# Kernel optimization log

Hardware: AMD Instinct MI355X
Metric: run time of the kernel (lower is better)

The kernel has to match this reference:

```python
import jax, jax.numpy as jnp
import numpy as np

NUM_HEADS = 16

def _rope_tables(seq_len, dim, dtype):
    # LongLlamaRotaryEmbedding: inv_freq = 1/10000^(2i/d), emb = cat(freqs, freqs)
    inv_freq = 1.0 / (10000.0 ** (jnp.arange(0, dim, 2, dtype=jnp.float32) / dim))
    t = jnp.arange(seq_len, dtype=jnp.float32)
    freqs = t[:, None] * inv_freq[None, :]            # [S, D/2]
    emb = jnp.concatenate([freqs, freqs], axis=-1)    # [S, D]
    return jnp.cos(emb).astype(dtype), jnp.sin(emb).astype(dtype)

def _rotate_half(x):
    x1, x2 = jnp.split(x, 2, axis=-1)
    return jnp.concatenate([-x2, x1], axis=-1)

def _rotate_one(x, cos, sin, pos):
    # x: [B,H,S,D]; pos: [B,S] int -> gather-indexed RoPE
    c = cos[pos][:, None, :, :]  # [B,1,S,D]
    s = sin[pos][:, None, :, :]
    return x * c + _rotate_half(x) * s

def setup_inputs() -> dict:
    key = jax.random.key(0)
    B, S, HID = 1, 4096, 2048
    ks = jax.random.split(key, 5)
    hidden_states = jax.random.normal(ks[0], (B, S, HID), dtype=jnp.float32)
    # causal additive mask [B,1,S,S]: 0 where allowed, large negative above diagonal
    causal = jnp.tril(jnp.ones((S, S), dtype=bool))
    attention_mask = jnp.where(causal, 0.0, -1e9).astype(jnp.float32)[None, None]
    attention_mask = jnp.broadcast_to(attention_mask, (B, 1, S, S))
    position_ids = jnp.broadcast_to(jnp.arange(S, dtype=jnp.int64), (B, S))
    scale = 0.02
    Wq = jax.random.normal(ks[1], (HID, HID), dtype=jnp.float32) * scale
    Wk = jax.random.normal(ks[2], (HID, HID), dtype=jnp.float32) * scale
    Wv = jax.random.normal(ks[3], (HID, HID), dtype=jnp.float32) * scale
    Wo = jax.random.normal(ks[4], (HID, HID), dtype=jnp.float32) * scale
    return {"hidden_states": hidden_states, "attention_mask": attention_mask,
            "position_ids": position_ids, "Wq": Wq, "Wk": Wk, "Wv": Wv, "Wo": Wo}

def reference(hidden_states, attention_mask, position_ids, Wq, Wk, Wv, Wo):
    B, S, HID = hidden_states.shape
    H = NUM_HEADS
    D = HID // H
    # QKV projections (torch Linear: y = x @ W.T), shaped [B,H,S,D]
    q = (hidden_states @ Wq.T).reshape(B, S, H, D).transpose(0, 2, 1, 3)
    k = (hidden_states @ Wk.T).reshape(B, S, H, D).transpose(0, 2, 1, 3)
    v = (hidden_states @ Wv.T).reshape(B, S, H, D).transpose(0, 2, 1, 3)
    kv_seq_len = k.shape[-2]
    cos, sin = _rope_tables(kv_seq_len, D, hidden_states.dtype)
    # rel_pos_ids = position_ids - min over seq (gather-indexed RoPE)
    rel = position_ids - jnp.min(position_ids, axis=-1, keepdims=True)
    q = _rotate_one(q, cos, sin, rel[:, -S:])
    k = _rotate_one(k, cos, sin, rel)
    scores = jnp.einsum('bhqd,bhkd->bhqk', q, k) / jnp.asarray(np.sqrt(D), hidden_states.dtype)
    scores = scores + attention_mask  # additive mask broadcast over heads
    attn = jax.nn.softmax(scores, axis=-1)
    out = jnp.einsum('bhqk,bhkd->bhqd', attn, v)
    out = out.transpose(0, 2, 1, 3).reshape(B, S, HID)
    return out @ Wo.T
```

## Files before the change

### kernel.cpp

```cpp
#include <hip/hip_runtime.h>
#include <stdint.h>

typedef uint16_t u16;
typedef __bf16 bf16x8 __attribute__((ext_vector_type(8)));
typedef float f32x4 __attribute__((ext_vector_type(4)));
typedef uint32_t u32x4 __attribute__((ext_vector_type(4)));

__device__ __forceinline__ u16 f2bf(float f) {
    uint32_t u = __builtin_bit_cast(uint32_t, f);
    u += 0x7fffu + ((u >> 16) & 1u);
    return (u16)(u >> 16);
}
__device__ __forceinline__ float bf2f(u16 h) {
    uint32_t u = ((uint32_t)h) << 16;
    return __builtin_bit_cast(float, u);
}

__global__ __launch_bounds__(256) void cvt_f32_bf16(const float* __restrict__ in,
                                                    u16* __restrict__ out, int n4) {
    int i = blockIdx.x * 256 + threadIdx.x;
    if (i >= n4) return;
    float4 v = ((const float4*)in)[i];
    u16 o[4] = { f2bf(v.x), f2bf(v.y), f2bf(v.z), f2bf(v.w) };
    *(uint64_t*)(out + 4 * (size_t)i) = *(const uint64_t*)o;
}

__global__ __launch_bounds__(256) void cvt_w4(const float* __restrict__ W0,
                                              const float* __restrict__ W1,
                                              const float* __restrict__ W2,
                                              const float* __restrict__ W3,
                                              u16* __restrict__ Wqkv,
                                              u16* __restrict__ Wob) {
    int b = blockIdx.x;
    int w = b >> 12;
    const float* in = (w == 0 ? W0 : w == 1 ? W1 : w == 2 ? W2 : W3);
    u16* out = (w < 3 ? Wqkv + (size_t)w * 4194304 : Wob);
    int i = (b & 4095) * 256 + threadIdx.x;
    float4 v = ((const float4*)in)[i];
    u16 o[4] = { f2bf(v.x), f2bf(v.y), f2bf(v.z), f2bf(v.w) };
    *(uint64_t*)(out + 4 * (size_t)i) = *(const uint64_t*)o;
}

__device__ __forceinline__ void gload16(const u16* g, u16* l) {
    __builtin_amdgcn_global_load_lds(
        (const __attribute__((address_space(1))) void*)g,
        (__attribute__((address_space(3))) void*)l, 16, 0, 0);
}

__global__ __launch_bounds__(512, 1) void gemm_qkv(const u16* __restrict__ A,
                                                   const u16* __restrict__ B,
                                                   u16* __restrict__ Cq,
                                                   int K) {
    __shared__ u16 As[2][16384];
    __shared__ u16 Bs[2][16384];
    const int tid  = threadIdx.x;
    const int wave = tid >> 6, lane = tid & 63;
    const int quad = lane >> 4, ln = lane & 15;
    const int wm = wave >> 2, wn = wave & 3;
    const int bm = blockIdx.x, bn = blockIdx.y;
    const int NT = K >> 6;
    const u16* Ab = A + (size_t)bm * 256 * K;
    const u16* Bb = B + (size_t)bn * 256 * K;
    const int lr  = lane >> 3;
    const int lc8 = ((lane & 7) ^ lr) * 8;
    const int sw  = ln & 7;
    const int cA0 = ((0 + quad) ^ sw) * 8;
    const int cA1 = ((4 + quad) ^ sw) * 8;

    f32x4 acc[8][4] = {};

    auto stage_a = [&](int t, int q) {
        int ch = q * 8 + wave;
        gload16(Ab + (size_t)(ch * 8 + lr) * K + t * 64 + lc8, &As[t & 1][ch * 512]);
    };
    auto stage_b = [&](int t, int q) {
        int ch = q * 8 + wave;
        gload16(Bb + (size_t)(ch * 8 + lr) * K + t * 64 + lc8, &Bs[t & 1][ch * 512]);
    };

    for (int q = 0; q < 4; q++) stage_a(0, q);
    for (int q = 0; q < 4; q++) stage_b(0, q);
    for (int q = 0; q < 4; q++) stage_a(1, q);
    asm volatile("s_waitcnt vmcnt(4)" ::: "memory");
    __builtin_amdgcn_s_barrier();

    for (int t = 0; t < NT; ++t) {
        const u16* Asb = As[t & 1];
        const u16* Bsb = Bs[t & 1];
        bf16x8 a0[8], a1[8], b0[4], b1[4];
#pragma unroll
        for (int i = 0; i < 8; i++)
            a0[i] = *(const bf16x8*)(Asb + (wm * 128 + i * 16 + ln) * 64 + cA0);
#pragma unroll
        for (int j = 0; j < 4; j++)
            b0[j] = *(const bf16x8*)(Bsb + (wn * 64 + j * 16 + ln) * 64 + cA0);
        if (t + 1 < NT) { stage_b(t + 1, 0); stage_b(t + 1, 1); }
        __builtin_amdgcn_s_barrier();
        asm volatile("s_waitcnt lgkmcnt(0)" ::: "memory");
        __builtin_amdgcn_s_setprio(1);
#pragma unroll
        for (int i = 0; i < 4; i++)
#pragma unroll
            for (int j = 0; j < 4; j++)
                acc[i][j] = __builtin_amdgcn_mfma_f32_16x16x32_bf16(a0[i], b0[j], acc[i][j], 0, 0, 0);
        __builtin_amdgcn_s_setprio(0);
        __builtin_amdgcn_s_barrier();
#pragma unroll
        for (int i = 0; i < 8; i++)
            a1[i] = *(const bf16x8*)(Asb + (wm * 128 + i * 16 + ln) * 64 + cA1);
        if (t + 1 < NT) { stage_b(t + 1, 2); stage_b(t + 1, 3); }
        __builtin_amdgcn_s_barrier();
        asm volatile("s_waitcnt lgkmcnt(0)" ::: "memory");
        __builtin_amdgcn_s_setprio(1);
#pragma unroll
        for (int i = 4; i < 8; i++)
#pragma unroll
            for (int j = 0; j < 4; j++)
                acc[i][j] = __builtin_amdgcn_mfma_f32_16x16x32_bf16(a0[i], b0[j], acc[i][j], 0, 0, 0);
        __builtin_amdgcn_s_setprio(0);
        __builtin_amdgcn_s_barrier();
#pragma unroll
        for (int j = 0; j < 4; j++)
            b1[j] = *(const bf16x8*)(Bsb + (wn * 64 + j * 16 + ln) * 64 + cA1);
        if (t + 2 < NT) { stage_a(t + 2, 0); stage_a(t + 2, 1); }
        __builtin_amdgcn_s_barrier();
        asm volatile("s_waitcnt lgkmcnt(0)" ::: "memory");
        __builtin_amdgcn_s_setprio(1);
#pragma unroll
        for (int i = 0; i < 4; i++)
#pragma unroll
            for (int j = 0; j < 4; j++)
                acc[i][j] = __builtin_amdgcn_mfma_f32_16x16x32_bf16(a1[i], b1[j], acc[i][j], 0, 0, 0);
        __builtin_amdgcn_s_setprio(0);
        __builtin_amdgcn_s_barrier();
        if (t + 2 < NT) { stage_a(t + 2, 2); stage_a(t + 2, 3); }
        __builtin_amdgcn_s_barrier();
        __builtin_amdgcn_s_setprio(1);
#pragma unroll
        for (int i = 4; i < 8; i++)
#pragma unroll
            for (int j = 0; j < 4; j++)
                acc[i][j] = __builtin_amdgcn_mfma_f32_16x16x32_bf16(a1[i], b1[j], acc[i][j], 0, 0, 0);
        __builtin_amdgcn_s_setprio(0);
        if (t + 2 < NT) asm volatile("s_waitcnt vmcnt(4)" ::: "memory");
        else            asm volatile("s_waitcnt vmcnt(0)" ::: "memory");
        __builtin_amdgcn_s_barrier();
    }
#pragma unroll
    for (int i = 0; i < 8; i++) {
        size_t row0 = (size_t)(bm * 256 + wm * 128 + i * 16 + quad * 4);
#pragma unroll
        for (int j = 0; j < 4; j++) {
            int n = bn * 256 + wn * 64 + j * 16 + ln;
            size_t off = ((size_t)(n >> 11) << 23) + (size_t)(n & 2047);
#pragma unroll
            for (int r = 0; r < 4; r++)
                Cq[off + (row0 + r) * 2048] = f2bf(acc[i][j][r]);
        }
    }
}

__global__ __launch_bounds__(256, 2) void gemm_o(const u16* __restrict__ A,
                                                 const u16* __restrict__ B,
                                                 float* __restrict__ C,
                                                 int K) {
    __shared__ u16 As[2][8192];
    __shared__ u16 Bs[2][8192];
    const int tid  = threadIdx.x;
    const int wave = tid >> 6, lane = tid & 63;
    const int quad = lane >> 4, ln = lane & 15;
    const int wm = (wave & 1) * 64, wn = (wave >> 1) * 64;
    const int bm = blockIdx.x, bn = blockIdx.y;
    const int NT = K >> 6;
    const u16* Ab = A + (size_t)bm * 128 * K;
    const u16* Bb = B + (size_t)bn * 128 * K;
    const int lr  = lane >> 3;
    const int lc8 = ((lane & 7) ^ lr) * 8;
    const int sw  = ln & 7;
    const int cA0 = ((0 + quad) ^ sw) * 8;
    const int cA1 = ((4 + quad) ^ sw) * 8;

    f32x4 acc[4][4] = {};

    auto stage_a = [&](int t, int q) {
        int ch = q * 4 + wave;
        gload16(Ab + (size_t)(ch * 8 + lr) * K + t * 64 + lc8, &As[t & 1][ch * 512]);
    };
    auto stage_b = [&](int t, int q) {
        int ch = q * 4 + wave;
        gload16(Bb + (size_t)(ch * 8 + lr) * K + t * 64 + lc8, &Bs[t & 1][ch * 512]);
    };

    for (int q = 0; q < 4; q++) stage_a(0, q);
    for (int q = 0; q < 4; q++) stage_b(0, q);
    for (int q = 0; q < 4; q++) stage_a(1, q);
    asm volatile("s_waitcnt vmcnt(4)" ::: "memory");
    __builtin_amdgcn_s_barrier();

    for (int t = 0; t < NT; ++t) {
        const u16* Asb = As[t & 1];
        const u16* Bsb = Bs[t & 1];
        bf16x8 a0[4], a1[4], b0[4], b1[4];
#pragma unroll
        for (int i = 0; i < 4; i++) {
            a0[i] = *(const bf16x8*)(Asb + (wm + i * 16 + ln) * 64 + cA0);
            b0[i] = *(const bf16x8*)(Bsb + (wn + i * 16 + ln) * 64 + cA0);
        }
        if (t + 1 < NT) { stage_b(t + 1, 0); stage_b(t + 1, 1); }
        __builtin_amdgcn_s_barrier();
        asm volatile("s_waitcnt lgkmcnt(0)" ::: "memory");
        __builtin_amdgcn_s_setprio(1);
#pragma unroll
        for (int i = 0; i < 2; i++)
#pragma unroll
            for (int j = 0; j < 4; j++)
                acc[i][j] = __builtin_amdgcn_mfma_f32_16x16x32_bf16(a0[i], b0[j], acc[i][j], 0, 0, 0);
        __builtin_amdgcn_s_setprio(0);
        __builtin_amdgcn_s_barrier();
#pragma unroll
        for (int i = 0; i < 4; i++) {
            a1[i] = *(const bf16x8*)(Asb + (wm + i * 16 + ln) * 64 + cA1);
            b1[i] = *(const bf16x8*)(Bsb + (wn + i * 16 + ln) * 64 + cA1);
        }
        if (t + 1 < NT) { stage_b(t + 1, 2); stage_b(t + 1, 3); }
        __builtin_amdgcn_s_barrier();
        asm volatile("s_waitcnt lgkmcnt(0)" ::: "memory");
        __builtin_amdgcn_s_setprio(1);
#pragma unroll
        for (int i = 2; i < 4; i++)
#pragma unroll
            for (int j = 0; j < 4; j++)
                acc[i][j] = __builtin_amdgcn_mfma_f32_16x16x32_bf16(a0[i], b0[j], acc[i][j], 0, 0, 0);
        __builtin_amdgcn_s_setprio(0);
        __builtin_amdgcn_s_barrier();
        if (t + 2 < NT) { stage_a(t + 2, 0); stage_a(t + 2, 1); }
        __builtin_amdgcn_s_barrier();
        __builtin_amdgcn_s_setprio(1);
#pragma unroll
        for (int i = 0; i < 2; i++)
#pragma unroll
            for (int j = 0; j < 4; j++)
                acc[i][j] = __builtin_amdgcn_mfma_f32_16x16x32_bf16(a1[i], b1[j], acc[i][j], 0, 0, 0);
        __builtin_amdgcn_s_setprio(0);
        __builtin_amdgcn_s_barrier();
        if (t + 2 < NT) { stage_a(t + 2, 2); stage_a(t + 2, 3); }
        __builtin_amdgcn_s_barrier();
        __builtin_amdgcn_s_setprio(1);
#pragma unroll
        for (int i = 2; i < 4; i++)
#pragma unroll
            for (int j = 0; j < 4; j++)
                acc[i][j] = __builtin_amdgcn_mfma_f32_16x16x32_bf16(a1[i], b1[j], acc[i][j], 0, 0, 0);
        __builtin_amdgcn_s_setprio(0);
        if (t + 2 < NT) asm volatile("s_waitcnt vmcnt(4)" ::: "memory");
        else            asm volatile("s_waitcnt vmcnt(0)" ::: "memory");
        __builtin_amdgcn_s_barrier();
    }
#pragma unroll
    for (int i = 0; i < 4; i++)
#pragma unroll
        for (int j = 0; j < 4; j++)
#pragma unroll
            for (int r = 0; r < 4; r++) {
                size_t row = (size_t)(bm * 128 + wm + i * 16 + quad * 4 + r);
                size_t col = (size_t)(bn * 128 + wn + j * 16 + ln);
                C[row * 2048 + col] = acc[i][j][r];
            }
}

__global__ __launch_bounds__(256) void rope_scale(u16* __restrict__ Qb,
                                                  u16* __restrict__ Kb) {
    const int j = threadIdx.x & 63;
    const int s = blockIdx.x * 4 + (threadIdx.x >> 6);
    float invf = exp2f((float)(-j) * 0.2076205059304601f);
    float th = (float)s * invf;
    float sn, cs;
    sincosf(th, &sn, &cs);
    const float QS = 0.08838834764831845f * 1.4426950408889634f;
    const float csq = cs * QS, snq = sn * QS;
    u16* qrow = Qb + (size_t)s * 2048 + j;
    u16* krow = Kb + (size_t)s * 2048 + j;
#pragma unroll
    for (int h = 0; h < 16; h++) {
        float x1 = bf2f(qrow[h * 128]);
        float x2 = bf2f(qrow[h * 128 + 64]);
        qrow[h * 128]      = f2bf(x1 * csq - x2 * snq);
        qrow[h * 128 + 64] = f2bf(x2 * csq + x1 * snq);
        float y1 = bf2f(krow[h * 128]);
        float y2 = bf2f(krow[h * 128 + 64]);
        krow[h * 128]      = f2bf(y1 * cs - y2 * sn);
        krow[h * 128 + 64] = f2bf(y2 * cs + y1 * sn);
    }
}

__global__ __launch_bounds__(256) void transpose_v(const u16* __restrict__ V,
                                                   u16* __restrict__ Vt) {
    __shared__ u16 T[64][136];
    const int h  = blockIdx.y;
    const int s0 = blockIdx.x * 64;
    const int tid = threadIdx.x;
    const int sr = tid >> 2, ck = (tid & 3) * 32;
    const u16* src = V + (size_t)(s0 + sr) * 2048 + h * 128 + ck;
    u32x4 v0 = *(const u32x4*)(src);
    u32x4 v1 = *(const u32x4*)(src + 8);
    u32x4 v2 = *(const u32x4*)(src + 16);
    u32x4 v3 = *(const u32x4*)(src + 24);
    *(u32x4*)&T[sr][ck]      = v0;
    *(u32x4*)&T[sr][ck + 8]  = v1;
    *(u32x4*)&T[sr][ck + 16] = v2;
    *(u32x4*)&T[sr][ck + 24] = v3;
    __syncthreads();
    const int d = tid >> 1, hs = (tid & 1) * 32;
    u16 tmp[32];
#pragma unroll
    for (int sidx = 0; sidx < 32; sidx++)
        tmp[sidx] = T[hs + sidx][d];
    u16* dst = Vt + ((size_t)h * 128 + d) * 4096 + s0 + hs;
    *(u32x4*)(dst)      = *(const u32x4*)(tmp);
    *(u32x4*)(dst + 8)  = *(const u32x4*)(tmp + 8);
    *(u32x4*)(dst + 16) = *(const u32x4*)(tmp + 16);
    *(u32x4*)(dst + 24) = *(const u32x4*)(tmp + 24);
}

__global__ __launch_bounds__(256, 3) void fattn(const u16* __restrict__ Qb,
                                                const u16* __restrict__ Kb,
                                                const u16* __restrict__ Vt,
                                                float* __restrict__ Oacc,
                                                float* __restrict__ Lacc) {
    __shared__ u16 Ks[2][32 * 128];
    __shared__ u16 Vs[2][128 * 32];
    __shared__ u16 Ps[128][40];
    const int tid  = threadIdx.x, wave = tid >> 6, lane = tid & 63;
    const int quad = lane >> 4, ln = lane & 15;
    const int h = blockIdx.x;
    const int y = blockIdx.y;
    int c, qt;
    if (y < 32)      { c = 0; qt = 31 - y; }
    else if (y < 56) { c = 1; qt = 63 - y; }
    else if (y < 72) { c = 2; qt = 87 - y; }
    else             { c = 3; qt = 103 - y; }
    const int q0 = qt * 128;
    const int nkt = min(32, 4 * qt + 4 - 32 * c);
    const int ktbase = 32 * c;

    const u16* Kp0 = Kb + h * 128;
    const u16* Vp0 = Vt + (size_t)h * 128 * 4096;

    bf16x8 aq[2][4];
    const u16* Qp = Qb + (size_t)q0 * 2048 + h * 128;
#pragma unroll
    for (int i = 0; i < 2; i++)
#pragma unroll
        for (int ks = 0; ks < 4; ks++)
            aq[i][ks] = *(const bf16x8*)(Qp + (size_t)(wave * 32 + i * 16 + ln) * 2048
                                         + ks * 32 + quad * 8);

    f32x4 o[2][8] = {};
    float lreg[2][4] = {};

    auto stage = [&](int kt, int b) {
        const u16* Kp = Kp0 + (size_t)(kt * 32) * 2048;
        const u16* Vp = Vp0 + kt * 32;
#pragma unroll
        for (int t = 0; t < 2; t++) {
            int p = (wave * 2 + t) * 64 + lane;
            int r = p >> 4, jc = (p & 15) ^ (r & 15);
            gload16(Kp + (size_t)r * 2048 + jc * 8, &Ks[b][(wave * 2 + t) * 512]);
        }
#pragma unroll
        for (int t = 0; t < 2; t++) {
            int p = (wave * 2 + t) * 64 + lane;
            int r = p >> 2, jc = (p & 3) ^ (r & 3);
            gload16(Vp + (size_t)r * 4096 + jc * 8, &Vs[b][(wave * 2 + t) * 512]);
        }
    };

    stage(ktbase, 0);
    for (int t = 0; t < nkt; t++) {
        __syncthreads();
        if (t + 1 < nkt) stage(ktbase + t + 1, (t + 1) & 1);
        const u16* Ksb = Ks[t & 1];
        const u16* Vsb = Vs[t & 1];

        f32x4 sc[2][2] = {};
        __builtin_amdgcn_s_setprio(1);
#pragma unroll
        for (int ks = 0; ks < 4; ks++)
#pragma unroll
            for (int j = 0; j < 2; j++) {
                int r = j * 16 + ln;
                bf16x8 bk = *(const bf16x8*)(Ksb + (size_t)(r * 16 + ((ks * 4 + quad) ^ ln)) * 8);
                sc[0][j] = __builtin_amdgcn_mfma_f32_16x16x32_bf16(aq[0][ks], bk, sc[0][j], 0, 0, 0);
                sc[1][j] = __builtin_amdgcn_mfma_f32_16x16x32_bf16(aq[1][ks], bk, sc[1][j], 0, 0, 0);
            }
        __builtin_amdgcn_s_setprio(0);
        const int kv0 = (ktbase + t) * 32;
        if (kv0 + 31 > q0 + wave * 32) {
#pragma unroll
            for (int j = 0; j < 2; j++) {
                int col = kv0 + j * 16 + ln;
#pragma unroll
                for (int i = 0; i < 2; i++)
#pragma unroll
                    for (int r = 0; r < 4; r++) {
                        int row = q0 + wave * 32 + i * 16 + quad * 4 + r;
                        if (col > row) sc[i][j][r] = -1e30f;
                    }
            }
        }
#pragma unroll
        for (int i = 0; i < 2; i++)
#pragma unroll
            for (int r = 0; r < 4; r++) {
                float p0 = __builtin_amdgcn_exp2f(sc[i][0][r]);
                float p1 = __builtin_amdgcn_exp2f(sc[i][1][r]);
                lreg[i][r] += p0 + p1;
                int row = wave * 32 + i * 16 + quad * 4 + r;
                Ps[row][ln]      = f2bf(p0);
                Ps[row][16 + ln] = f2bf(p1);
            }
        bf16x8 pa0 = *(const bf16x8*)&Ps[wave * 32 + ln][quad * 8];
        bf16x8 pa1 = *(const bf16x8*)&Ps[wave * 32 + 16 + ln][quad * 8];
        __builtin_amdgcn_s_setprio(1);
#pragma unroll
        for (int n = 0; n < 8; n++) {
            int rv = n * 16 + ln;
            bf16x8 vb = *(const bf16x8*)(Vsb + (size_t)(rv * 4 + (quad ^ (ln & 3))) * 8);
            o[0][n] = __builtin_amdgcn_mfma_f32_16x16x32_bf16(pa0, vb, o[0][n], 0, 0, 0);
            o[1][n] = __builtin_amdgcn_mfma_f32_16x16x32_bf16(pa1, vb, o[1][n], 0, 0, 0);
        }
        __builtin_amdgcn_s_setprio(0);
    }
    float* Op = Oacc + (size_t)(q0 + wave * 32) * 2048 + h * 128;
#pragma unroll
    for (int i = 0; i < 2; i++)
#pragma unroll
        for (int r = 0; r < 4; r++) {
            float l = lreg[i][r];
            l += __shfl_xor(l, 1);
            l += __shfl_xor(l, 2);
            l += __shfl_xor(l, 4);
            l += __shfl_xor(l, 8);
            int row = i * 16 + quad * 4 + r;
            if (ln == 0)
                unsafeAtomicAdd(&Lacc[(size_t)(q0 + wave * 32 + row) * 16 + h], l);
#pragma unroll
            for (int n = 0; n < 8; n++)
                unsafeAtomicAdd(&Op[(size_t)row * 2048 + n * 16 + ln], o[i][n][r]);
        }
}

__global__ __launch_bounds__(256) void attn_norm(const float* __restrict__ Oacc,
                                                 const float* __restrict__ Lacc,
                                                 u16* __restrict__ attn) {
    int i = blockIdx.x * 256 + threadIdx.x;
    int s  = i >> 9;
    int c4 = (i & 511) * 4;
    int h  = c4 >> 7;
    float inv = 1.0f / Lacc[(size_t)s * 16 + h];
    float4 v = ((const float4*)(Oacc + (size_t)s * 2048))[i & 511];
    u16 o[4] = { f2bf(v.x * inv), f2bf(v.y * inv), f2bf(v.z * inv), f2bf(v.w * inv) };
    *(uint64_t*)(attn + (size_t)s * 2048 + c4) = *(const uint64_t*)o;
}

extern "C" void kernel_launch(void* const* d_in, const int* in_sizes, int n_in,
                              void* d_out, int out_size, void* d_ws, size_t ws_size,
                              hipStream_t stream) {
    const float* hs = (const float*)d_in[0];
    const float* Wq = (const float*)d_in[3];
    const float* Wk = (const float*)d_in[4];
    const float* Wv = (const float*)d_in[5];
    const float* Wo = (const float*)d_in[6];

    char* ws = (char*)d_ws;
    u16* Xb   = (u16*)ws;
    u16* Wob  = (u16*)(ws + (size_t)16777216);
    u16* Qb   = (u16*)(ws + (size_t)25165824);
    u16* Kb   = (u16*)(ws + (size_t)41943040);
    u16* Vb   = (u16*)(ws + (size_t)58720256);
    u16* Wqkv = (u16*)(ws + (size_t)75497472);
    u16* Vtg  = (u16*)(ws + (size_t)100663296);
    float* Oacc = (float*)(ws + (size_t)58720256);
    float* Lacc = (float*)(ws + (size_t)92274688);
    u16* attn = Xb;

    cvt_f32_bf16<<<8192, 256, 0, stream>>>(hs, Xb, 2097152);
    cvt_w4<<<16384, 256, 0, stream>>>(Wq, Wk, Wv, Wo, Wqkv, Wob);

    gemm_qkv<<<dim3(16, 24), 512, 0, stream>>>(Xb, Wqkv, Qb, 2048);
    rope_scale<<<1024, 256, 0, stream>>>(Qb, Kb);
    transpose_v<<<dim3(64, 16), 256, 0, stream>>>(Vb, Vtg);
    hipMemsetAsync(Oacc, 0, 33816576, stream);
    fattn<<<dim3(16, 80), 256, 0, stream>>>(Qb, Kb, Vtg, Oacc, Lacc);
    attn_norm<<<8192, 256, 0, stream>>>(Oacc, Lacc, attn);
    gemm_o<<<dim3(32, 16), 256, 0, stream>>>(attn, Wob, (float*)d_out, 2048);
}
```

Measured before the change: 496.3 us.

## Remap GEMM blocks per XCD and restructure QKV prefetch schedule with fewer registers

```diff
diff --git a/kernel.cpp b/kernel.cpp
--- a/kernel.cpp
+++ b/kernel.cpp
@@ -57,7 +57,10 @@
     const int wave = tid >> 6, lane = tid & 63;
     const int quad = lane >> 4, ln = lane & 15;
     const int wm = wave >> 2, wn = wave & 3;
-    const int bm = blockIdx.x, bn = blockIdx.y;
+    const int id   = blockIdx.x + blockIdx.y * 16;
+    const int xcd  = id & 7, slot = id >> 3;
+    const int bn   = xcd * 3 + (slot >> 4);
+    const int bm   = slot & 15;
     const int NT = K >> 6;
     const u16* Ab = A + (size_t)bm * 256 * K;
     const u16* Bb = B + (size_t)bn * 256 * K;
@@ -80,21 +83,21 @@
 
     for (int q = 0; q < 4; q++) stage_a(0, q);
     for (int q = 0; q < 4; q++) stage_b(0, q);
-    for (int q = 0; q < 4; q++) stage_a(1, q);
-    asm volatile("s_waitcnt vmcnt(4)" ::: "memory");
+    if (NT > 1) { stage_b(1, 0); stage_b(1, 1); }
+    if (NT > 1) asm volatile("s_waitcnt vmcnt(2)" ::: "memory");
+    else        asm volatile("s_waitcnt vmcnt(0)" ::: "memory");
     __builtin_amdgcn_s_barrier();
 
     for (int t = 0; t < NT; ++t) {
         const u16* Asb = As[t & 1];
         const u16* Bsb = Bs[t & 1];
-        bf16x8 a0[8], a1[8], b0[4], b1[4];
-#pragma unroll
-        for (int i = 0; i < 8; i++)
-            a0[i] = *(const bf16x8*)(Asb + (wm * 128 + i * 16 + ln) * 64 + cA0);
-#pragma unroll
-        for (int j = 0; j < 4; j++)
-            b0[j] = *(const bf16x8*)(Bsb + (wn * 64 + j * 16 + ln) * 64 + cA0);
-        if (t + 1 < NT) { stage_b(t + 1, 0); stage_b(t + 1, 1); }
+        bf16x8 a[4], b0[4], b1[4];
+#pragma unroll
+        for (int i = 0; i < 4; i++) {
+            a[i]  = *(const bf16x8*)(Asb + (wm * 128 + i * 16 + ln) * 64 + cA0);
+            b0[i] = *(const bf16x8*)(Bsb + (wn * 64 + i * 16 + ln) * 64 + cA0);
+        }
+        if (t + 1 < NT) { stage_b(t + 1, 2); stage_b(t + 1, 3); }
         __builtin_amdgcn_s_barrier();
         asm volatile("s_waitcnt lgkmcnt(0)" ::: "memory");
         __builtin_amdgcn_s_setprio(1);
@@ -102,27 +105,29 @@
         for (int i = 0; i < 4; i++)
 #pragma unroll
             for (int j = 0; j < 4; j++)
-                acc[i][j] = __builtin_amdgcn_mfma_f32_16x16x32_bf16(a0[i], b0[j], acc[i][j], 0, 0, 0);
-        __builtin_amdgcn_s_setprio(0);
-        __builtin_amdgcn_s_barrier();
-#pragma unroll
-        for (int i = 0; i < 8; i++)
-            a1[i] = *(const bf16x8*)(Asb + (wm * 128 + i * 16 + ln) * 64 + cA1);
-        if (t + 1 < NT) { stage_b(t + 1, 2); stage_b(t + 1, 3); }
+                acc[i][j] = __builtin_amdgcn_mfma_f32_16x16x32_bf16(a[i], b0[j], acc[i][j], 0, 0, 0);
+        __builtin_amdgcn_s_setprio(0);
+        __builtin_amdgcn_s_barrier();
+#pragma unroll
+        for (int i = 0; i < 4; i++)
+            a[i] = *(const bf16x8*)(Asb + (wm * 128 + (4 + i) * 16 + ln) * 64 + cA0);
+        if (t + 1 < NT) { stage_a(t + 1, 0); stage_a(t + 1, 1); }
         __builtin_amdgcn_s_barrier();
         asm volatile("s_waitcnt lgkmcnt(0)" ::: "memory");
         __builtin_amdgcn_s_setprio(1);
 #pragma unroll
-        for (int i = 4; i < 8; i++)
-#pragma unroll
-            for (int j = 0; j < 4; j++)
-                acc[i][j] = __builtin_amdgcn_mfma_f32_16x16x32_bf16(a0[i], b0[j], acc[i][j], 0, 0, 0);
-        __builtin_amdgcn_s_setprio(0);
-        __builtin_amdgcn_s_barrier();
-#pragma unroll
-        for (int j = 0; j < 4; j++)
-            b1[j] = *(const bf16x8*)(Bsb + (wn * 64 + j * 16 + ln) * 64 + cA1);
-        if (t + 2 < NT) { stage_a(t + 2, 0); stage_a(t + 2, 1); }
+        for (int i = 0; i < 4; i++)
+#pragma unroll
+            for (int j = 0; j < 4; j++)
+                acc[4 + i][j] = __builtin_amdgcn_mfma_f32_16x16x32_bf16(a[i], b0[j], acc[4 + i][j], 0, 0, 0);
+        __builtin_amdgcn_s_setprio(0);
+        __builtin_amdgcn_s_barrier();
+#pragma unroll
+        for (int i = 0; i < 4; i++) {
+            a[i]  = *(const bf16x8*)(Asb + (wm * 128 + i * 16 + ln) * 64 + cA1);
+            b1[i] = *(const bf16x8*)(Bsb + (wn * 64 + i * 16 + ln) * 64 + cA1);
+        }
+        if (t + 1 < NT) { stage_a(t + 1, 2); stage_a(t + 1, 3); }
         __builtin_amdgcn_s_barrier();
         asm volatile("s_waitcnt lgkmcnt(0)" ::: "memory");
         __builtin_amdgcn_s_setprio(1);
@@ -130,19 +135,23 @@
         for (int i = 0; i < 4; i++)
 #pragma unroll
             for (int j = 0; j < 4; j++)
-                acc[i][j] = __builtin_amdgcn_mfma_f32_16x16x32_bf16(a1[i], b1[j], acc[i][j], 0, 0, 0);
-        __builtin_amdgcn_s_setprio(0);
-        __builtin_amdgcn_s_barrier();
-        if (t + 2 < NT) { stage_a(t + 2, 2); stage_a(t + 2, 3); }
-        __builtin_amdgcn_s_barrier();
-        __builtin_amdgcn_s_setprio(1);
-#pragma unroll
-        for (int i = 4; i < 8; i++)
-#pragma unroll
-            for (int j = 0; j < 4; j++)
-                acc[i][j] = __builtin_amdgcn_mfma_f32_16x16x32_bf16(a1[i], b1[j], acc[i][j], 0, 0, 0);
-        __builtin_amdgcn_s_setprio(0);
-        if (t + 2 < NT) asm volatile("s_waitcnt vmcnt(4)" ::: "memory");
+                acc[i][j] = __builtin_amdgcn_mfma_f32_16x16x32_bf16(a[i], b1[j], acc[i][j], 0, 0, 0);
+        __builtin_amdgcn_s_setprio(0);
+        __builtin_amdgcn_s_barrier();
+#pragma unroll
+        for (int i = 0; i < 4; i++)
+            a[i] = *(const bf16x8*)(Asb + (wm * 128 + (4 + i) * 16 + ln) * 64 + cA1);
+        if (t + 2 < NT) { stage_b(t + 2, 0); stage_b(t + 2, 1); }
+        __builtin_amdgcn_s_barrier();
+        asm volatile("s_waitcnt lgkmcnt(0)" ::: "memory");
+        __builtin_amdgcn_s_setprio(1);
+#pragma unroll
+        for (int i = 0; i < 4; i++)
+#pragma unroll
+            for (int j = 0; j < 4; j++)
+                acc[4 + i][j] = __builtin_amdgcn_mfma_f32_16x16x32_bf16(a[i], b1[j], acc[4 + i][j], 0, 0, 0);
+        __builtin_amdgcn_s_setprio(0);
+        if (t + 2 < NT) asm volatile("s_waitcnt vmcnt(2)" ::: "memory");
         else            asm volatile("s_waitcnt vmcnt(0)" ::: "memory");
         __builtin_amdgcn_s_barrier();
     }
@@ -170,7 +179,10 @@
     const int wave = tid >> 6, lane = tid & 63;
     const int quad = lane >> 4, ln = lane & 15;
     const int wm = (wave & 1) * 64, wn = (wave >> 1) * 64;
-    const int bm = blockIdx.x, bn = blockIdx.y;
+    const int id   = blockIdx.x + blockIdx.y * 32;
+    const int xcd  = id & 7, slot = id >> 3;
+    const int bn   = xcd * 2 + (slot >> 5);
+    const int bm   = slot & 31;
     const int NT = K >> 6;
     const u16* Ab = A + (size_t)bm * 128 * K;
     const u16* Bb = B + (size_t)bn * 128 * K;
```

Result: no change. 500.3 us (+0.8%).
